# Performance work log

Hardware: AMD Instinct MI355X
Metric: run time of the kernel (lower is better)

Reference implementation:

```python
import jax, jax.numpy as jnp
import numpy as np

N_NODES = 20000
N_EDGES = 640000
DIM_NODE = 256
DIM_EDGE = 128
N_CENTERS = 64
DIM_HIDDEN = 128


def setup_inputs() -> dict:
    key = jax.random.key(0)
    ks = jax.random.split(key, 12)
    inp = {
        "node_h": jax.random.normal(ks[0], (N_NODES, DIM_NODE), dtype=jnp.float32),
        "edge_h": jax.random.normal(ks[1], (N_EDGES, DIM_EDGE), dtype=jnp.float32),
        "dist": jax.random.normal(ks[2], (N_EDGES, N_CENTERS), dtype=jnp.float32),
        "src": jax.random.randint(ks[3], (N_EDGES,), 0, N_NODES, dtype=jnp.int32),
        "dst": jax.random.randint(ks[4], (N_EDGES,), 0, N_NODES, dtype=jnp.int32),
        # learned params (nn.Linear: y = x @ W.T + b; we store W already transposed)
        "W_node": jax.random.normal(ks[5], (DIM_NODE, DIM_HIDDEN), dtype=jnp.float32) / np.sqrt(DIM_NODE),
        "b_node": jnp.zeros((DIM_HIDDEN,), dtype=jnp.float32),
        "W_edge": jax.random.normal(ks[6], (DIM_EDGE, DIM_HIDDEN), dtype=jnp.float32) / np.sqrt(DIM_EDGE),
        "b_edge": jnp.zeros((DIM_HIDDEN,), dtype=jnp.float32),
        "W_dist": jax.random.normal(ks[7], (N_CENTERS, DIM_HIDDEN), dtype=jnp.float32) / np.sqrt(N_CENTERS),
        "b_dist": jnp.zeros((DIM_HIDDEN,), dtype=jnp.float32),
        "W_comb": jax.random.normal(ks[8], (2 * DIM_HIDDEN, DIM_NODE), dtype=jnp.float32) / np.sqrt(2 * DIM_HIDDEN),
    }
    return inp


def reference(node_h, edge_h, dist, src, dst,
              W_node, b_node, W_edge, b_edge, W_dist, b_dist, W_comb):
    # fc_node is per-node: compute once on [N, dim_node], then gather per edge
    node_proj = node_h @ W_node + b_node            # [N, H]
    m1 = node_proj[src] * (dist @ W_dist + b_dist)  # [E, H]
    m2 = edge_h @ W_edge + b_edge                   # [E, H]
    m = jnp.tanh(jnp.concatenate([m1, m2], axis=1) @ W_comb)  # [E, dim_node]
    # scatter-sum into destination nodes (DGL reduce: mailbox sum)
    h = jax.ops.segment_sum(m, dst, num_segments=N_NODES)     # [N, dim_node]
    # per-node L2 normalization (norm=True)
    h = h / jnp.linalg.norm(h, axis=1, keepdims=True)
    return h
```

## Files before the change

kernel.cpp:

```cpp
#include <hip/hip_runtime.h>
#include <hip/hip_bf16.h>
#include <math.h>

typedef __attribute__((ext_vector_type(4))) float fx4;
typedef __attribute__((ext_vector_type(8))) short bx8;
typedef __attribute__((ext_vector_type(4))) short bx4;

#define DEV static __device__ __forceinline__
#define N_NODES 20000
#define N_EDGES 640000

DEV unsigned short f2bf(float f){
  __hip_bfloat16 h = __float2bfloat16(f);
  return *(unsigned short*)&h;
}
DEV float bf2f(unsigned short h){
  union { float f; unsigned u; } a; a.u = ((unsigned)h) << 16;
  return a.f;
}
DEV float fast_tanh(float x){
  float t = __expf(2.0f * x);
  return 1.0f - 2.0f * __builtin_amdgcn_rcpf(t + 1.0f);
}
DEV bx8 cvt8(fx4 a, fx4 b){
  bx8 r;
  r[0]=(short)f2bf(a[0]); r[1]=(short)f2bf(a[1]); r[2]=(short)f2bf(a[2]); r[3]=(short)f2bf(a[3]);
  r[4]=(short)f2bf(b[0]); r[5]=(short)f2bf(b[1]); r[6]=(short)f2bf(b[2]); r[7]=(short)f2bf(b[3]);
  return r;
}

__global__ __launch_bounds__(256)
void prep_kernel(const float* __restrict__ Wn, const float* __restrict__ Wd,
                 unsigned short* __restrict__ WnP, unsigned short* __restrict__ WdP)
{
  int t = blockIdx.x * 256 + threadIdx.x;
  if (t >= 40960) return;
  const float* W; unsigned short* P; int i, ks, nblk;
  if (t < 32768) { W=Wn; P=WnP; i=t;        ks=(i>>9)&7; nblk=i>>12; }
  else           { W=Wd; P=WdP; i=t-32768;  ks=(i>>9)&1; nblk=i>>10; }
  int j    = i & 7;
  int lane = (i >> 3) & 63;
  int k = ks*32 + (lane>>4)*8 + j;
  int n = nblk*16 + (lane&15);
  P[i] = f2bf(W[k*128 + n]);
}

__global__ __launch_bounds__(256)
void prep2_kernel(const float* __restrict__ We, const float* __restrict__ Wc,
                  const float* __restrict__ be,
                  unsigned short* __restrict__ WctP, unsigned short* __restrict__ WeffP,
                  float* __restrict__ ceff)
{
  int t = blockIdx.x * 256 + threadIdx.x;
  if (t < 32768){
    int i=t, j=i&7, lane=(i>>3)&63, ks=(i>>9)&3, nblk=i>>11;
    int k = ks*32 + (lane>>4)*8 + j;
    int n = nblk*16 + (lane&15);
    WctP[i] = f2bf(Wc[k*256 + n]);
  } else if (t < 65536){
    int i=t-32768, j=i&7, lane=(i>>3)&63, ks=(i>>9)&3, nblk=i>>11;
    int k = ks*32 + (lane>>4)*8 + j;
    int n = nblk*16 + (lane&15);
    float s = 0.f;
    for (int h = 0; h < 128; ++h)
      s += We[k*128 + h] * Wc[(128+h)*256 + n];
    WeffP[i] = f2bf(s);
  } else if (t < 65792){
    int n = t - 65536;
    float s = 0.f;
    for (int h = 0; h < 128; ++h)
      s += be[h] * Wc[(128+h)*256 + n];
    ceff[n] = s;
  }
}

__global__ __launch_bounds__(256)
void hist_kernel(const int* __restrict__ dst, int* __restrict__ cnt)
{
  int e = blockIdx.x * 256 + threadIdx.x;
  if (e < N_EDGES) atomicAdd(&cnt[dst[e]], 1);
}

__global__ __launch_bounds__(1024)
void scan_kernel(const int* __restrict__ cnt, int* __restrict__ fill)
{
  __shared__ int wsum[16];
  __shared__ int carry_s;
  const int t = threadIdx.x, lane = t & 63, w = t >> 6;
  if (t == 0) carry_s = 0;
  __syncthreads();
  for (int c = 0; c < 20; ++c){
    int i = c*1024 + t;
    int v = (i < N_NODES) ? cnt[i] : 0;
    int x = v;
#pragma unroll
    for (int s = 1; s < 64; s <<= 1){
      int u = __shfl_up(x, s, 64);
      if (lane >= s) x += u;
    }
    if (lane == 63) wsum[w] = x;
    __syncthreads();
    if (w == 0 && lane < 16){
      int y = wsum[lane];
#pragma unroll
      for (int s = 1; s < 16; s <<= 1){
        int u = __shfl_up(y, s, 64);
        if (lane >= s) y += u;
      }
      wsum[lane] = y;
    }
    __syncthreads();
    int wbase = (w == 0) ? 0 : wsum[w-1];
    int excl = carry_s + wbase + x - v;
    if (i < N_NODES) fill[i] = excl;
    __syncthreads();
    if (t == 1023) carry_s = excl + v;
    __syncthreads();
  }
}

__global__ __launch_bounds__(256)
void scatter_kernel(const int* __restrict__ dst, int* __restrict__ fill,
                    int* __restrict__ perm, int* __restrict__ dstS)
{
  int e = blockIdx.x * 256 + threadIdx.x;
  if (e < N_EDGES){
    int d = dst[e];
    int pos = atomicAdd(&fill[d], 1);
    perm[pos] = e;
    dstS[pos] = d;
  }
}

__global__ __launch_bounds__(64)
void node_proj_kernel(const float* __restrict__ node_h, const unsigned short* __restrict__ WnP,
                      const float* __restrict__ b_node, unsigned short* __restrict__ npj)
{
  __shared__ unsigned short sN[16 * 264];
  const int lane = threadIdx.x;
  const int lr = lane & 15, lq = lane >> 4;
  const long r0 = (long)blockIdx.x * 16;

  const fx4* g = (const fx4*)(node_h + r0 * 256);
#pragma unroll
  for (int i = 0; i < 16; ++i){
    int idx = lane + 64 * i;
    int r = idx >> 6, c4 = idx & 63;
    fx4 v = g[idx];
    bx4 b;
    b[0]=(short)f2bf(v[0]); b[1]=(short)f2bf(v[1]); b[2]=(short)f2bf(v[2]); b[3]=(short)f2bf(v[3]);
    *(bx4*)&sN[r*264 + c4*4] = b;
  }
  __syncthreads();

  fx4 acc[8];
#pragma unroll
  for (int n = 0; n < 8; ++n) acc[n] = (fx4){0.f,0.f,0.f,0.f};
#pragma unroll
  for (int ks = 0; ks < 8; ++ks){
    bx8 a = *(const bx8*)&sN[lr*264 + ks*32 + lq*8];
#pragma unroll
    for (int n = 0; n < 8; ++n){
      bx8 b = *(const bx8*)&WnP[((n*8 + ks)*64 + lane)*8];
      acc[n] = __builtin_amdgcn_mfma_f32_16x16x32_bf16(a, b, acc[n], 0, 0, 0);
    }
  }
#pragma unroll
  for (int n = 0; n < 8; ++n){
    float bias = b_node[n*16 + lr];
#pragma unroll
    for (int j = 0; j < 4; ++j)
      npj[(r0 + lq*4 + j)*128 + n*16 + lr] = f2bf(acc[n][j] + bias);
  }
}

__global__ __launch_bounds__(256, 4)
void edge_kernel(const float* __restrict__ edge_h, const float* __restrict__ dist,
                 const int* __restrict__ src,
                 const int* __restrict__ perm, const int* __restrict__ dstS,
                 const unsigned short* __restrict__ npj,
                 const unsigned short* __restrict__ WdP, const float* __restrict__ b_dist,
                 const unsigned short* __restrict__ WctP, const unsigned short* __restrict__ WeffP,
                 const float* __restrict__ ceff,
                 float* __restrict__ hacc)
{
  __shared__ unsigned short sX[4][16*136];
  __shared__ unsigned short sE[4][16*136];

  const int tid  = threadIdx.x;
  const int w    = tid >> 6;
  const int lane = tid & 63;
  const int lr   = lane & 15;
  const int lq   = lane >> 4;
  const int c32  = lane & 31;
  const long e0  = (long)blockIdx.x * 64;

  int vPerm = 0, vSrc = 0;
  if (lane < 16){
    int p = perm[e0 + w*16 + lane];
    vPerm = p;
    vSrc  = src[p];
  }
  const int vDst = dstS[e0 + lane];
  const int pRow = __shfl(vPerm, lr);

  fx4 rE[8];
#pragma unroll
  for (int i = 0; i < 8; ++i){
    int r = (lane >> 5) + 2*i;
    int p = __shfl(vPerm, r);
    rE[i] = *(const fx4*)(edge_h + (long)p*128 + c32*4);
  }

  bx4 rN[8];
#pragma unroll
  for (int i = 0; i < 8; ++i){
    int r = (lane >> 5) + 2*i;
    int s = __shfl(vSrc, r);
    rN[i] = *(const bx4*)(npj + (long)s*128 + c32*4);
  }

  const float* dp = dist + (long)pRow*64 + lq*8;
  fx4 d0 = *(const fx4*)(dp);
  fx4 d1 = *(const fx4*)(dp + 4);
  fx4 d2 = *(const fx4*)(dp + 32);
  fx4 d3 = *(const fx4*)(dp + 36);

#pragma unroll
  for (int i = 0; i < 8; ++i){
    int r = (lane >> 5) + 2*i;
    bx4 cv;
    cv[0]=(short)f2bf(rE[i][0]); cv[1]=(short)f2bf(rE[i][1]);
    cv[2]=(short)f2bf(rE[i][2]); cv[3]=(short)f2bf(rE[i][3]);
    *(bx4*)&sE[w][r*136 + c32*4] = cv;
  }

  {
    bx8 a0 = cvt8(d0, d1);
    bx8 a1 = cvt8(d2, d3);
    fx4 facc[8];
#pragma unroll
    for (int n = 0; n < 8; ++n){
      float bdv = b_dist[n*16 + lr];
      facc[n] = (fx4){bdv, bdv, bdv, bdv};
    }
#pragma unroll
    for (int n = 0; n < 8; ++n){
      bx8 b = *(const bx8*)&WdP[((n*2 + 0)*64 + lane)*8];
      facc[n] = __builtin_amdgcn_mfma_f32_16x16x32_bf16(a0, b, facc[n], 0, 0, 0);
    }
#pragma unroll
    for (int n = 0; n < 8; ++n){
      bx8 b = *(const bx8*)&WdP[((n*2 + 1)*64 + lane)*8];
      facc[n] = __builtin_amdgcn_mfma_f32_16x16x32_bf16(a1, b, facc[n], 0, 0, 0);
    }
#pragma unroll
    for (int n = 0; n < 8; ++n)
#pragma unroll
      for (int j = 0; j < 4; ++j)
        sX[w][(lq*4 + j)*136 + n*16 + lr] = f2bf(facc[n][j]);
  }

#pragma unroll
  for (int i = 0; i < 8; ++i){
    int r = (lane >> 5) + 2*i;
    bx4 dp4 = *(const bx4*)&sX[w][r*136 + c32*4];
    bx4 o;
#pragma unroll
    for (int k = 0; k < 4; ++k)
      o[k] = (short)f2bf( bf2f((unsigned short)rN[i][k]) * bf2f((unsigned short)dp4[k]) );
    *(bx4*)&sX[w][r*136 + c32*4] = o;
  }
  __syncthreads();

  int up = __shfl_up(vDst, 1);
  bool head = (lane == 0) || (up != vDst);
  const unsigned long long mhead = __ballot(head);

#pragma unroll
  for (int h = 0; h < 2; ++h){
    fx4 acc[4][2];
#pragma unroll
    for (int rt = 0; rt < 4; ++rt)
#pragma unroll
      for (int n = 0; n < 2; ++n) acc[rt][n] = (fx4){0.f,0.f,0.f,0.f};
#pragma unroll
    for (int ks = 0; ks < 4; ++ks){
      bx8 a[4], b[2];
#pragma unroll
      for (int rt = 0; rt < 4; ++rt)
        a[rt] = *(const bx8*)&sX[rt][lr*136 + ks*32 + lq*8];
#pragma unroll
      for (int n = 0; n < 2; ++n)
        b[n] = *(const bx8*)&WctP[(((4*w + 2*h + n)*4 + ks)*64 + lane)*8];
#pragma unroll
      for (int rt = 0; rt < 4; ++rt)
#pragma unroll
        for (int n = 0; n < 2; ++n)
          acc[rt][n] = __builtin_amdgcn_mfma_f32_16x16x32_bf16(a[rt], b[n], acc[rt][n], 0, 0, 0);
    }
#pragma unroll
    for (int ks = 0; ks < 4; ++ks){
      bx8 a[4], b[2];
#pragma unroll
      for (int rt = 0; rt < 4; ++rt)
        a[rt] = *(const bx8*)&sE[rt][lr*136 + ks*32 + lq*8];
#pragma unroll
      for (int n = 0; n < 2; ++n)
        b[n] = *(const bx8*)&WeffP[(((4*w + 2*h + n)*4 + ks)*64 + lane)*8];
#pragma unroll
      for (int rt = 0; rt < 4; ++rt)
#pragma unroll
        for (int n = 0; n < 2; ++n)
          acc[rt][n] = __builtin_amdgcn_mfma_f32_16x16x32_bf16(a[rt], b[n], acc[rt][n], 0, 0, 0);
    }

    float ce0 = ceff[(4*w + 2*h + 0)*16 + lr];
    float ce1 = ceff[(4*w + 2*h + 1)*16 + lr];
#pragma unroll
    for (int rt = 0; rt < 4; ++rt)
#pragma unroll
      for (int j = 0; j < 4; ++j){
        acc[rt][0][j] = fast_tanh(acc[rt][0][j] + ce0);
        acc[rt][1][j] = fast_tanh(acc[rt][1][j] + ce1);
      }

    unsigned long long m = mhead;
    while (m){
      int lo = __ffsll((unsigned long long)m) - 1;
      m &= m - 1;
      int hi = m ? (__ffsll((unsigned long long)m) - 1) : 64;
      int d  = __shfl(vDst, lo);
      float s0 = 0.f, s1 = 0.f;
#pragma unroll
      for (int rt = 0; rt < 4; ++rt)
#pragma unroll
        for (int j = 0; j < 4; ++j){
          int row = rt*16 + lq*4 + j;
          float msk = (row >= lo && row < hi) ? 1.f : 0.f;
          s0 += msk * acc[rt][0][j];
          s1 += msk * acc[rt][1][j];
        }
      s0 += __shfl_xor(s0, 16); s0 += __shfl_xor(s0, 32);
      s1 += __shfl_xor(s1, 16); s1 += __shfl_xor(s1, 32);
      if (lq < 2){
        float v = (lq == 0) ? s0 : s1;
        float* p = &hacc[(long)d*256 + (4*w + 2*h + lq)*16 + lr];
        if (lo == 0 || hi == 64) atomicAdd(p, v);
        else                     *p = v;
      }
    }
  }
}

__global__ __launch_bounds__(256)
void norm_kernel(float* __restrict__ h)
{
  int row  = blockIdx.x * 4 + (threadIdx.x >> 6);
  int lane = threadIdx.x & 63;
  fx4 v = *(const fx4*)&h[(long)row*256 + lane*4];
  float s = v[0]*v[0] + v[1]*v[1] + v[2]*v[2] + v[3]*v[3];
#pragma unroll
  for (int off = 32; off > 0; off >>= 1) s += __shfl_xor(s, off);
  float inv = (s > 0.f) ? 1.0f / sqrtf(s) : 0.f;
  v[0]*=inv; v[1]*=inv; v[2]*=inv; v[3]*=inv;
  *(fx4*)&h[(long)row*256 + lane*4] = v;
}

extern "C" void kernel_launch(void* const* d_in, const int* in_sizes, int n_in,
                              void* d_out, int out_size, void* d_ws, size_t ws_size,
                              hipStream_t stream)
{
  const float* node_h = (const float*)d_in[0];
  const float* edge_h = (const float*)d_in[1];
  const float* dist   = (const float*)d_in[2];
  const int*   src    = (const int*)d_in[3];
  const int*   dst    = (const int*)d_in[4];
  const float* W_node = (const float*)d_in[5];
  const float* b_node = (const float*)d_in[6];
  const float* W_edge = (const float*)d_in[7];
  const float* b_edge = (const float*)d_in[8];
  const float* W_dist = (const float*)d_in[9];
  const float* b_dist = (const float*)d_in[10];
  const float* W_comb = (const float*)d_in[11];

  char* ws = (char*)d_ws;
  unsigned short* npj   = (unsigned short*)ws;
  unsigned short* WnP   = (unsigned short*)(ws + 5120000);
  unsigned short* WdP   = (unsigned short*)(ws + 5185536);
  unsigned short* WctP  = (unsigned short*)(ws + 5201920);
  unsigned short* WeffP = (unsigned short*)(ws + 5267456);
  float*          ceff  = (float*)(ws + 5332992);
  int* cnt  = (int*)(ws + 5334016);
  int* fill = (int*)(ws + 5414016);
  int* perm = (int*)(ws + 5494016);
  int* dstS = (int*)(ws + 8054016);

  float* hacc = (float*)d_out;

  hipMemsetAsync(hacc, 0, (size_t)N_NODES * 256 * sizeof(float), stream);
  hipMemsetAsync(cnt, 0, (size_t)N_NODES * sizeof(int), stream);

  prep_kernel<<<160, 256, 0, stream>>>(W_node, W_dist, WnP, WdP);
  prep2_kernel<<<257, 256, 0, stream>>>(W_edge, W_comb, b_edge, WctP, WeffP, ceff);
  hist_kernel<<<2500, 256, 0, stream>>>(dst, cnt);
  scan_kernel<<<1, 1024, 0, stream>>>(cnt, fill);
  scatter_kernel<<<2500, 256, 0, stream>>>(dst, fill, perm, dstS);
  node_proj_kernel<<<1250, 64, 0, stream>>>(node_h, WnP, b_node, npj);
  edge_kernel<<<10000, 256, 0, stream>>>(edge_h, dist, src, perm, dstS, npj,
                                         WdP, b_dist, WctP, WeffP, ceff, hacc);
  norm_kernel<<<5000, 256, 0, stream>>>(hacc);
}
```

Measured before the change: 379.6 us.

## Make edge kernel loop over four tiles, prefetch dist, parallelize scan, merge prep kernels

The edge kernel now processes 256 edges per block in a loop of four 64-edge tiles. It loads perm and src indices once and prefetches the next tile's dist rows while the current tile computes, which lowers the block count and overlaps loads with work. The single-block serial scan is replaced by a three-kernel block scan, and the two weight-prep kernels are merged into one launch. The trade-offs are less grid parallelism, extra register pressure from the prefetched rows, and two more small launches for the scan.

```diff
diff --git a/kernel.cpp b/kernel.cpp
--- a/kernel.cpp
+++ b/kernel.cpp
@@ -30,43 +30,33 @@
 }
 
 __global__ __launch_bounds__(256)
-void prep_kernel(const float* __restrict__ Wn, const float* __restrict__ Wd,
-                 unsigned short* __restrict__ WnP, unsigned short* __restrict__ WdP)
-{
-  int t = blockIdx.x * 256 + threadIdx.x;
-  if (t >= 40960) return;
-  const float* W; unsigned short* P; int i, ks, nblk;
-  if (t < 32768) { W=Wn; P=WnP; i=t;        ks=(i>>9)&7; nblk=i>>12; }
-  else           { W=Wd; P=WdP; i=t-32768;  ks=(i>>9)&1; nblk=i>>10; }
-  int j    = i & 7;
-  int lane = (i >> 3) & 63;
-  int k = ks*32 + (lane>>4)*8 + j;
-  int n = nblk*16 + (lane&15);
-  P[i] = f2bf(W[k*128 + n]);
-}
-
-__global__ __launch_bounds__(256)
-void prep2_kernel(const float* __restrict__ We, const float* __restrict__ Wc,
-                  const float* __restrict__ be,
-                  unsigned short* __restrict__ WctP, unsigned short* __restrict__ WeffP,
-                  float* __restrict__ ceff)
+void prep_all_kernel(const float* __restrict__ Wn, const float* __restrict__ Wd,
+                     const float* __restrict__ We, const float* __restrict__ Wc,
+                     const float* __restrict__ be,
+                     unsigned short* __restrict__ WnP, unsigned short* __restrict__ WdP,
+                     unsigned short* __restrict__ WctP, unsigned short* __restrict__ WeffP,
+                     float* __restrict__ ceff)
 {
   int t = blockIdx.x * 256 + threadIdx.x;
   if (t < 32768){
-    int i=t, j=i&7, lane=(i>>3)&63, ks=(i>>9)&3, nblk=i>>11;
-    int k = ks*32 + (lane>>4)*8 + j;
-    int n = nblk*16 + (lane&15);
-    WctP[i] = f2bf(Wc[k*256 + n]);
-  } else if (t < 65536){
-    int i=t-32768, j=i&7, lane=(i>>3)&63, ks=(i>>9)&3, nblk=i>>11;
+    int i=t, j=i&7, lane=(i>>3)&63, ks=(i>>9)&7, nblk=i>>12;
+    WnP[i] = f2bf(Wn[(ks*32 + (lane>>4)*8 + j)*128 + nblk*16 + (lane&15)]);
+  } else if (t < 40960){
+    int i=t-32768, j=i&7, lane=(i>>3)&63, ks=(i>>9)&1, nblk=i>>10;
+    WdP[i] = f2bf(Wd[(ks*32 + (lane>>4)*8 + j)*128 + nblk*16 + (lane&15)]);
+  } else if (t < 73728){
+    int i=t-40960, j=i&7, lane=(i>>3)&63, ks=(i>>9)&3, nblk=i>>11;
+    WctP[i] = f2bf(Wc[(ks*32 + (lane>>4)*8 + j)*256 + nblk*16 + (lane&15)]);
+  } else if (t < 106496){
+    int i=t-73728, j=i&7, lane=(i>>3)&63, ks=(i>>9)&3, nblk=i>>11;
     int k = ks*32 + (lane>>4)*8 + j;
     int n = nblk*16 + (lane&15);
     float s = 0.f;
     for (int h = 0; h < 128; ++h)
       s += We[k*128 + h] * Wc[(128+h)*256 + n];
     WeffP[i] = f2bf(s);
-  } else if (t < 65792){
-    int n = t - 65536;
+  } else if (t < 106752){
+    int n = t - 106496;
     float s = 0.f;
     for (int h = 0; h < 128; ++h)
       s += be[h] * Wc[(128+h)*256 + n];
@@ -82,41 +72,55 @@
 }
 
 __global__ __launch_bounds__(1024)
-void scan_kernel(const int* __restrict__ cnt, int* __restrict__ fill)
+void scanA_kernel(const int* __restrict__ cnt, int* __restrict__ fill, int* __restrict__ bsum)
 {
   __shared__ int wsum[16];
-  __shared__ int carry_s;
   const int t = threadIdx.x, lane = t & 63, w = t >> 6;
-  if (t == 0) carry_s = 0;
+  int i = blockIdx.x * 1024 + t;
+  int v = (i < N_NODES) ? cnt[i] : 0;
+  int x = v;
+#pragma unroll
+  for (int s = 1; s < 64; s <<= 1){
+    int u = __shfl_up(x, s, 64);
+    if (lane >= s) x += u;
+  }
+  if (lane == 63) wsum[w] = x;
   __syncthreads();
-  for (int c = 0; c < 20; ++c){
-    int i = c*1024 + t;
-    int v = (i < N_NODES) ? cnt[i] : 0;
-    int x = v;
-#pragma unroll
-    for (int s = 1; s < 64; s <<= 1){
-      int u = __shfl_up(x, s, 64);
-      if (lane >= s) x += u;
-    }
-    if (lane == 63) wsum[w] = x;
-    __syncthreads();
-    if (w == 0 && lane < 16){
-      int y = wsum[lane];
-#pragma unroll
-      for (int s = 1; s < 16; s <<= 1){
-        int u = __shfl_up(y, s, 64);
-        if (lane >= s) y += u;
-      }
-      wsum[lane] = y;
-    }
-    __syncthreads();
-    int wbase = (w == 0) ? 0 : wsum[w-1];
-    int excl = carry_s + wbase + x - v;
-    if (i < N_NODES) fill[i] = excl;
-    __syncthreads();
-    if (t == 1023) carry_s = excl + v;
-    __syncthreads();
-  }
+  if (w == 0 && lane < 16){
+    int y = wsum[lane];
+#pragma unroll
+    for (int s = 1; s < 16; s <<= 1){
+      int u = __shfl_up(y, s, 64);
+      if (lane >= s) y += u;
+    }
+    wsum[lane] = y;
+  }
+  __syncthreads();
+  int wbase = (w == 0) ? 0 : wsum[w-1];
+  int excl = wbase + x - v;
+  if (i < N_NODES) fill[i] = excl;
+  if (t == 1023) bsum[blockIdx.x] = excl + v;
+}
+
+__global__ __launch_bounds__(64)
+void scanB_kernel(int* __restrict__ bsum)
+{
+  int lane = threadIdx.x;
+  int v = (lane < 20) ? bsum[lane] : 0;
+  int x = v;
+#pragma unroll
+  for (int s = 1; s < 32; s <<= 1){
+    int u = __shfl_up(x, s, 64);
+    if (lane >= s) x += u;
+  }
+  if (lane < 20) bsum[lane] = x - v;
+}
+
+__global__ __launch_bounds__(1024)
+void scanC_kernel(int* __restrict__ fill, const int* __restrict__ bsum)
+{
+  int i = blockIdx.x * 1024 + threadIdx.x;
+  if (i < N_NODES) fill[i] += bsum[blockIdx.x];
 }
 
 __global__ __launch_bounds__(256)
@@ -193,163 +197,171 @@
   const int lr   = lane & 15;
   const int lq   = lane >> 4;
   const int c32  = lane & 31;
-  const long e0  = (long)blockIdx.x * 64;
-
-  int vPerm = 0, vSrc = 0;
-  if (lane < 16){
-    int p = perm[e0 + w*16 + lane];
-    vPerm = p;
-    vSrc  = src[p];
-  }
-  const int vDst = dstS[e0 + lane];
-  const int pRow = __shfl(vPerm, lr);
-
-  fx4 rE[8];
-#pragma unroll
-  for (int i = 0; i < 8; ++i){
-    int r = (lane >> 5) + 2*i;
-    int p = __shfl(vPerm, r);
-    rE[i] = *(const fx4*)(edge_h + (long)p*128 + c32*4);
-  }
-
-  bx4 rN[8];
-#pragma unroll
-  for (int i = 0; i < 8; ++i){
-    int r = (lane >> 5) + 2*i;
-    int s = __shfl(vSrc, r);
-    rN[i] = *(const bx4*)(npj + (long)s*128 + c32*4);
-  }
-
-  const float* dp = dist + (long)pRow*64 + lq*8;
-  fx4 d0 = *(const fx4*)(dp);
-  fx4 d1 = *(const fx4*)(dp + 4);
-  fx4 d2 = *(const fx4*)(dp + 32);
-  fx4 d3 = *(const fx4*)(dp + 36);
-
-#pragma unroll
-  for (int i = 0; i < 8; ++i){
-    int r = (lane >> 5) + 2*i;
-    bx4 cv;
-    cv[0]=(short)f2bf(rE[i][0]); cv[1]=(short)f2bf(rE[i][1]);
-    cv[2]=(short)f2bf(rE[i][2]); cv[3]=(short)f2bf(rE[i][3]);
-    *(bx4*)&sE[w][r*136 + c32*4] = cv;
-  }
-
+  const long eb  = (long)blockIdx.x * 256;
+
+  const int vPermAll = perm[eb + (long)(lane >> 4)*64 + w*16 + (lane & 15)];
+  const int vSrcAll  = src[vPermAll];
+
+  fx4 pD0, pD1, pD2, pD3;
   {
-    bx8 a0 = cvt8(d0, d1);
-    bx8 a1 = cvt8(d2, d3);
-    fx4 facc[8];
-#pragma unroll
-    for (int n = 0; n < 8; ++n){
-      float bdv = b_dist[n*16 + lr];
-      facc[n] = (fx4){bdv, bdv, bdv, bdv};
-    }
-#pragma unroll
-    for (int n = 0; n < 8; ++n){
-      bx8 b = *(const bx8*)&WdP[((n*2 + 0)*64 + lane)*8];
-      facc[n] = __builtin_amdgcn_mfma_f32_16x16x32_bf16(a0, b, facc[n], 0, 0, 0);
-    }
-#pragma unroll
-    for (int n = 0; n < 8; ++n){
-      bx8 b = *(const bx8*)&WdP[((n*2 + 1)*64 + lane)*8];
-      facc[n] = __builtin_amdgcn_mfma_f32_16x16x32_bf16(a1, b, facc[n], 0, 0, 0);
-    }
-#pragma unroll
-    for (int n = 0; n < 8; ++n)
-#pragma unroll
-      for (int j = 0; j < 4; ++j)
-        sX[w][(lq*4 + j)*136 + n*16 + lr] = f2bf(facc[n][j]);
-  }
-
-#pragma unroll
-  for (int i = 0; i < 8; ++i){
-    int r = (lane >> 5) + 2*i;
-    bx4 dp4 = *(const bx4*)&sX[w][r*136 + c32*4];
-    bx4 o;
-#pragma unroll
-    for (int k = 0; k < 4; ++k)
-      o[k] = (short)f2bf( bf2f((unsigned short)rN[i][k]) * bf2f((unsigned short)dp4[k]) );
-    *(bx4*)&sX[w][r*136 + c32*4] = o;
-  }
-  __syncthreads();
-
-  int up = __shfl_up(vDst, 1);
-  bool head = (lane == 0) || (up != vDst);
-  const unsigned long long mhead = __ballot(head);
-
-#pragma unroll
-  for (int h = 0; h < 2; ++h){
-    fx4 acc[4][2];
-#pragma unroll
-    for (int rt = 0; rt < 4; ++rt)
-#pragma unroll
-      for (int n = 0; n < 2; ++n) acc[rt][n] = (fx4){0.f,0.f,0.f,0.f};
-#pragma unroll
-    for (int ks = 0; ks < 4; ++ks){
-      bx8 a[4], b[2];
+    int pr = __shfl(vPermAll, lr);
+    const float* dp = dist + (long)pr*64 + lq*8;
+    pD0 = *(const fx4*)(dp);      pD1 = *(const fx4*)(dp + 4);
+    pD2 = *(const fx4*)(dp + 32); pD3 = *(const fx4*)(dp + 36);
+  }
+
+  for (int t = 0; t < 4; ++t){
+    const int vDst = dstS[eb + t*64 + lane];
+
+    fx4 rE[8];
+#pragma unroll
+    for (int i = 0; i < 8; ++i){
+      int r = (lane >> 5) + 2*i;
+      int p = __shfl(vPermAll, t*16 + r);
+      rE[i] = *(const fx4*)(edge_h + (long)p*128 + c32*4);
+    }
+    bx4 rN[8];
+#pragma unroll
+    for (int i = 0; i < 8; ++i){
+      int r = (lane >> 5) + 2*i;
+      int s = __shfl(vSrcAll, t*16 + r);
+      rN[i] = *(const bx4*)(npj + (long)s*128 + c32*4);
+    }
+
+    bx8 a0 = cvt8(pD0, pD1);
+    bx8 a1 = cvt8(pD2, pD3);
+    if (t < 3){
+      int prn = __shfl(vPermAll, (t+1)*16 + lr);
+      const float* dp = dist + (long)prn*64 + lq*8;
+      pD0 = *(const fx4*)(dp);      pD1 = *(const fx4*)(dp + 4);
+      pD2 = *(const fx4*)(dp + 32); pD3 = *(const fx4*)(dp + 36);
+    }
+
+#pragma unroll
+    for (int g = 0; g < 2; ++g){
+      fx4 facc[4];
+#pragma unroll
+      for (int n = 0; n < 4; ++n){
+        float bv = b_dist[(g*4 + n)*16 + lr];
+        facc[n] = (fx4){bv, bv, bv, bv};
+      }
+#pragma unroll
+      for (int n = 0; n < 4; ++n){
+        bx8 bf = *(const bx8*)&WdP[(((g*4 + n)*2 + 0)*64 + lane)*8];
+        facc[n] = __builtin_amdgcn_mfma_f32_16x16x32_bf16(a0, bf, facc[n], 0, 0, 0);
+      }
+#pragma unroll
+      for (int n = 0; n < 4; ++n){
+        bx8 bf = *(const bx8*)&WdP[(((g*4 + n)*2 + 1)*64 + lane)*8];
+        facc[n] = __builtin_amdgcn_mfma_f32_16x16x32_bf16(a1, bf, facc[n], 0, 0, 0);
+      }
+#pragma unroll
+      for (int n = 0; n < 4; ++n)
+#pragma unroll
+        for (int j = 0; j < 4; ++j)
+          sX[w][(lq*4 + j)*136 + (g*4 + n)*16 + lr] = f2bf(facc[n][j]);
+    }
+
+#pragma unroll
+    for (int i = 0; i < 8; ++i){
+      int r = (lane >> 5) + 2*i;
+      bx4 dp4 = *(const bx4*)&sX[w][r*136 + c32*4];
+      bx4 o;
+#pragma unroll
+      for (int k = 0; k < 4; ++k)
+        o[k] = (short)f2bf( bf2f((unsigned short)rN[i][k]) * bf2f((unsigned short)dp4[k]) );
+      *(bx4*)&sX[w][r*136 + c32*4] = o;
+    }
+
+#pragma unroll
+    for (int i = 0; i < 8; ++i){
+      int r = (lane >> 5) + 2*i;
+      bx4 cv;
+      cv[0]=(short)f2bf(rE[i][0]); cv[1]=(short)f2bf(rE[i][1]);
+      cv[2]=(short)f2bf(rE[i][2]); cv[3]=(short)f2bf(rE[i][3]);
+      *(bx4*)&sE[w][r*136 + c32*4] = cv;
+    }
+    __syncthreads();
+
+    int up = __shfl_up(vDst, 1);
+    bool head = (lane == 0) || (up != vDst);
+    const unsigned long long mhead = __ballot(head);
+
+#pragma unroll
+    for (int h = 0; h < 2; ++h){
+      fx4 acc[4][2];
 #pragma unroll
       for (int rt = 0; rt < 4; ++rt)
-        a[rt] = *(const bx8*)&sX[rt][lr*136 + ks*32 + lq*8];
-#pragma unroll
-      for (int n = 0; n < 2; ++n)
-        b[n] = *(const bx8*)&WctP[(((4*w + 2*h + n)*4 + ks)*64 + lane)*8];
+#pragma unroll
+        for (int n = 0; n < 2; ++n) acc[rt][n] = (fx4){0.f,0.f,0.f,0.f};
+#pragma unroll
+      for (int ks = 0; ks < 4; ++ks){
+        bx8 a[4], b[2];
+#pragma unroll
+        for (int rt = 0; rt < 4; ++rt)
+          a[rt] = *(const bx8*)&sX[rt][lr*136 + ks*32 + lq*8];
+#pragma unroll
+        for (int n = 0; n < 2; ++n)
+          b[n] = *(const bx8*)&WctP[(((4*w + 2*h + n)*4 + ks)*64 + lane)*8];
+#pragma unroll
+        for (int rt = 0; rt < 4; ++rt)
+#pragma unroll
+          for (int n = 0; n < 2; ++n)
+            acc[rt][n] = __builtin_amdgcn_mfma_f32_16x16x32_bf16(a[rt], b[n], acc[rt][n], 0, 0, 0);
+      }
+#pragma unroll
+      for (int ks = 0; ks < 4; ++ks){
+        bx8 a[4], b[2];
+#pragma unroll
+        for (int rt = 0; rt < 4; ++rt)
+          a[rt] = *(const bx8*)&sE[rt][lr*136 + ks*32 + lq*8];
+#pragma unroll
+        for (int n = 0; n < 2; ++n)
+          b[n] = *(const bx8*)&WeffP[(((4*w + 2*h + n)*4 + ks)*64 + lane)*8];
+#pragma unroll
+        for (int rt = 0; rt < 4; ++rt)
+#pragma unroll
+          for (int n = 0; n < 2; ++n)
+            acc[rt][n] = __builtin_amdgcn_mfma_f32_16x16x32_bf16(a[rt], b[n], acc[rt][n], 0, 0, 0);
+      }
+
+      float ce0 = ceff[(4*w + 2*h + 0)*16 + lr];
+      float ce1 = ceff[(4*w + 2*h + 1)*16 + lr];
 #pragma unroll
       for (int rt = 0; rt < 4; ++rt)
 #pragma unroll
-        for (int n = 0; n < 2; ++n)
-          acc[rt][n] = __builtin_amdgcn_mfma_f32_16x16x32_bf16(a[rt], b[n], acc[rt][n], 0, 0, 0);
-    }
-#pragma unroll
-    for (int ks = 0; ks < 4; ++ks){
-      bx8 a[4], b[2];
-#pragma unroll
-      for (int rt = 0; rt < 4; ++rt)
-        a[rt] = *(const bx8*)&sE[rt][lr*136 + ks*32 + lq*8];
-#pragma unroll
-      for (int n = 0; n < 2; ++n)
-        b[n] = *(const bx8*)&WeffP[(((4*w + 2*h + n)*4 + ks)*64 + lane)*8];
-#pragma unroll
-      for (int rt = 0; rt < 4; ++rt)
-#pragma unroll
-        for (int n = 0; n < 2; ++n)
-          acc[rt][n] = __builtin_amdgcn_mfma_f32_16x16x32_bf16(a[rt], b[n], acc[rt][n], 0, 0, 0);
-    }
-
-    float ce0 = ceff[(4*w + 2*h + 0)*16 + lr];
-    float ce1 = ceff[(4*w + 2*h + 1)*16 + lr];
-#pragma unroll
-    for (int rt = 0; rt < 4; ++rt)
-#pragma unroll
-      for (int j = 0; j < 4; ++j){
-        acc[rt][0][j] = fast_tanh(acc[rt][0][j] + ce0);
-        acc[rt][1][j] = fast_tanh(acc[rt][1][j] + ce1);
-      }
-
-    unsigned long long m = mhead;
-    while (m){
-      int lo = __ffsll((unsigned long long)m) - 1;
-      m &= m - 1;
-      int hi = m ? (__ffsll((unsigned long long)m) - 1) : 64;
-      int d  = __shfl(vDst, lo);
-      float s0 = 0.f, s1 = 0.f;
-#pragma unroll
-      for (int rt = 0; rt < 4; ++rt)
-#pragma unroll
         for (int j = 0; j < 4; ++j){
-          int row = rt*16 + lq*4 + j;
-          float msk = (row >= lo && row < hi) ? 1.f : 0.f;
-          s0 += msk * acc[rt][0][j];
-          s1 += msk * acc[rt][1][j];
+          acc[rt][0][j] = fast_tanh(acc[rt][0][j] + ce0);
+          acc[rt][1][j] = fast_tanh(acc[rt][1][j] + ce1);
         }
-      s0 += __shfl_xor(s0, 16); s0 += __shfl_xor(s0, 32);
-      s1 += __shfl_xor(s1, 16); s1 += __shfl_xor(s1, 32);
-      if (lq < 2){
-        float v = (lq == 0) ? s0 : s1;
-        float* p = &hacc[(long)d*256 + (4*w + 2*h + lq)*16 + lr];
-        if (lo == 0 || hi == 64) atomicAdd(p, v);
-        else                     *p = v;
-      }
-    }
+
+      unsigned long long m = mhead;
+      while (m){
+        int lo = __ffsll((unsigned long long)m) - 1;
+        m &= m - 1;
+        int hi = m ? (__ffsll((unsigned long long)m) - 1) : 64;
+        int d  = __shfl(vDst, lo);
+        float s0 = 0.f, s1 = 0.f;
+#pragma unroll
+        for (int rt = 0; rt < 4; ++rt)
+#pragma unroll
+          for (int j = 0; j < 4; ++j){
+            int row = rt*16 + lq*4 + j;
+            float msk = (row >= lo && row < hi) ? 1.f : 0.f;
+            s0 += msk * acc[rt][0][j];
+            s1 += msk * acc[rt][1][j];
+          }
+        s0 += __shfl_xor(s0, 16); s0 += __shfl_xor(s0, 32);
+        s1 += __shfl_xor(s1, 16); s1 += __shfl_xor(s1, 32);
+        if (lq < 2){
+          float v = (lq == 0) ? s0 : s1;
+          float* p = &hacc[(long)d*256 + (4*w + 2*h + lq)*16 + lr];
+          if (lo == 0 || hi == 64) atomicAdd(p, v);
+          else                     *p = v;
+        }
+      }
+    }
+    __syncthreads();
   }
 }
 
@@ -395,19 +407,22 @@
   int* fill = (int*)(ws + 5414016);
   int* perm = (int*)(ws + 5494016);
   int* dstS = (int*)(ws + 8054016);
+  int* bsum = (int*)(ws + 10614016);
 
   float* hacc = (float*)d_out;
 
   hipMemsetAsync(hacc, 0, (size_t)N_NODES * 256 * sizeof(float), stream);
   hipMemsetAsync(cnt, 0, (size_t)N_NODES * sizeof(int), stream);
 
-  prep_kernel<<<160, 256, 0, stream>>>(W_node, W_dist, WnP, WdP);
-  prep2_kernel<<<257, 256, 0, stream>>>(W_edge, W_comb, b_edge, WctP, WeffP, ceff);
+  prep_all_kernel<<<417, 256, 0, stream>>>(W_node, W_dist, W_edge, W_comb, b_edge,
+                                           WnP, WdP, WctP, WeffP, ceff);
   hist_kernel<<<2500, 256, 0, stream>>>(dst, cnt);
-  scan_kernel<<<1, 1024, 0, stream>>>(cnt, fill);
+  scanA_kernel<<<20, 1024, 0, stream>>>(cnt, fill, bsum);
+  scanB_kernel<<<1, 64, 0, stream>>>(bsum);
+  scanC_kernel<<<20, 1024, 0, stream>>>(fill, bsum);
   scatter_kernel<<<2500, 256, 0, stream>>>(dst, fill, perm, dstS);
   node_proj_kernel<<<1250, 64, 0, stream>>>(node_h, WnP, b_node, npj);
-  edge_kernel<<<10000, 256, 0, stream>>>(edge_h, dist, src, perm, dstS, npj,
-                                         WdP, b_dist, WctP, WeffP, ceff, hacc);
+  edge_kernel<<<2500, 256, 0, stream>>>(edge_h, dist, src, perm, dstS, npj,
+                                        WdP, b_dist, WctP, WeffP, ceff, hacc);
   norm_kernel<<<5000, 256, 0, stream>>>(hacc);
 }
```

Measured after the change: 832.3 us. 119% more time.
